# Kernel tuning notes

Hardware: AMD Instinct MI355X
Metric: run time of the kernel (lower is better)

The kernel has to match this reference:

```python
import jax, jax.numpy as jnp
import numpy as np

B, N, C = 1, 2048, 1024
H, D = 16, 64          # num_heads, head_dim
S = 8                  # number of frames; tokens per frame = N // S
NEG_INF = jnp.float32(-1e30)  # stand-in for -inf, numerically safe under jit


def setup_inputs() -> dict:
    key = jax.random.key(0)
    ks = jax.random.split(key, 8)
    x = jax.random.normal(ks[0], (B, N, C), dtype=jnp.float32)
    # tokens grouped contiguously by frame (sorted frame ids)
    frame_ids = jnp.repeat(jnp.arange(S, dtype=jnp.int32), N // S)
    is_hub = jax.random.bernoulli(ks[1], 0.05, (N,))
    adj = jax.random.bernoulli(ks[2], 0.25, (S, S))
    adj = adj.at[jnp.arange(S), jnp.arange(S)].set(True)  # frames always see self
    frame_bias = jax.random.normal(ks[3], (S, S), dtype=jnp.float32) * 0.1
    Wqkv = jax.random.normal(ks[4], (C, 3 * C), dtype=jnp.float32) * 0.02
    bqkv = jnp.zeros((3 * C,), dtype=jnp.float32)
    Wproj = jax.random.normal(ks[5], (C, C), dtype=jnp.float32) * 0.02
    bproj = jnp.zeros((C,), dtype=jnp.float32)
    return {"x": x, "frame_ids": frame_ids, "is_hub": is_hub, "adj": adj,
            "frame_bias": frame_bias, "Wqkv": Wqkv, "bqkv": bqkv,
            "Wproj": Wproj, "bproj": bproj}


def reference(x, frame_ids, is_hub, adj, frame_bias, Wqkv, bqkv, Wproj, bproj):
    # qkv projection: (B,N,3C) -> (3,B,H,N,D)
    qkv = (x @ Wqkv + bqkv).reshape(B, N, 3, H, D).transpose(2, 0, 3, 1, 4)
    q, k, v = qkv[0], qkv[1], qkv[2]

    # flex_attention: scores scaled by 1/sqrt(D) BEFORE score_mod
    scores = jnp.einsum("bhnd,bhmd->bhnm", q, k) * (D ** -0.5)

    # score_mod, vectorized over all (qi,kj) pairs:
    fi = frame_ids                                   # (N,)
    allow = adj[fi][:, fi]                           # (N,N) frame adjacency per token pair
    diff_frame = fi[:, None] != fi[None, :]
    hub_block = diff_frame & (is_hub[:, None] | is_hub[None, :])
    allow = allow & ~hub_block                       # mask_hub_tokens=True
    bias = frame_bias[fi][:, fi]                     # soft_mask=True: add frame-level bias

    scores = jnp.where(allow, scores + bias, NEG_INF)  # broadcast over (b,h)
    attn = jax.nn.softmax(scores, axis=-1)
    out = jnp.einsum("bhnm,bhmd->bhnd", attn, v)
    out = out.transpose(0, 2, 1, 3).reshape(B, N, C)
    return out @ Wproj + bproj
```

## Files before the change

### kernel.cpp

```cpp
#include <hip/hip_runtime.h>

#define NTOK 2048
#define CDIM 1024
#define NHEAD 16
#define HDIM 64
#define NFRM 8
#define FTOK 256

typedef unsigned short ushort;
typedef __attribute__((ext_vector_type(8))) short short8;
typedef __attribute__((ext_vector_type(8))) ushort ushort8;
typedef __attribute__((ext_vector_type(4))) ushort ushort4v;
typedef __attribute__((ext_vector_type(4))) float floatx4;

__device__ __forceinline__ ushort f2bf(float f) {
    unsigned int u = __float_as_uint(f);
    return (ushort)((u + 0x7fffu + ((u >> 16) & 1u)) >> 16);
}

__device__ __forceinline__ void gload_lds16(const void* g, void* l) {
    __builtin_amdgcn_global_load_lds(
        (const __attribute__((address_space(1))) unsigned int*)(uintptr_t)g,
        (__attribute__((address_space(3))) unsigned int*)(unsigned int)(uintptr_t)l,
        16, 0, 0);
}

__global__ __launch_bounds__(256)
void prep_kernel(const float* __restrict__ x, ushort* __restrict__ xb,
                 const float* __restrict__ Wqkv, ushort* __restrict__ wqkvT,
                 const float* __restrict__ Wproj, ushort* __restrict__ wprojT)
{
    __shared__ ushort LT[64][72];
    const int b = blockIdx.x, t = threadIdx.x;

    if (b < 2048) {
        int i = b * 256 + t;
        float4 f = ((const float4*)x)[i];
        ushort4v o = { f2bf(f.x), f2bf(f.y), f2bf(f.z), f2bf(f.w) };
        ((ushort4v*)xb)[i] = o;
        return;
    }

    const float* W; ushort* WT; int K, N, n0, k0;
    if (b < 2816) { int idx = b - 2048; W = Wqkv;  WT = wqkvT;  K = 1024; N = 3072;
                    n0 = (idx % 48) * 64; k0 = (idx / 48) * 64; }
    else          { int idx = b - 2816; W = Wproj; WT = wprojT; K = 1024; N = 1024;
                    n0 = (idx & 15) * 64; k0 = (idx >> 4) * 64; }

    const int kr = t >> 4, nc = t & 15;
#pragma unroll
    for (int i = 0; i < 4; ++i) {
        int k = kr + i * 16;
        float4 w4 = *(const float4*)(W + (size_t)(k0 + k) * N + n0 + nc * 4);
        LT[nc*4+0][k] = f2bf(w4.x);
        LT[nc*4+1][k] = f2bf(w4.y);
        LT[nc*4+2][k] = f2bf(w4.z);
        LT[nc*4+3][k] = f2bf(w4.w);
    }
    __syncthreads();
    const int n = t >> 2;
#pragma unroll
    for (int half = 0; half < 2; ++half) {
        int kc = (t & 3) + 4 * half;
        ushort8 v = *(const ushort8*)&LT[n][kc * 8];
        *(ushort8*)(WT + (size_t)(n0 + n) * K + k0 + kc * 8) = v;
    }
}

__global__ __launch_bounds__(256)
void vtrans_kernel(const ushort* __restrict__ v, ushort* __restrict__ vT)
{
    __shared__ ushort LT[64][72];
    const int t = threadIdx.x, h = blockIdx.y, n0 = blockIdx.x * 64;
    {
        const int tok = t >> 2;
#pragma unroll
        for (int half = 0; half < 2; ++half) {
            int dc = (t & 3) + 4 * half;
            ushort8 v8 = *(const ushort8*)(v + ((size_t)h * NTOK + n0 + tok) * HDIM + dc * 8);
#pragma unroll
            for (int j = 0; j < 8; ++j) LT[dc*8 + j][tok] = v8[j];
        }
    }
    __syncthreads();
    {
        const int d = t >> 2;
#pragma unroll
        for (int half = 0; half < 2; ++half) {
            int tc = (t & 3) + 4 * half;
            ushort8 o8 = *(const ushort8*)&LT[d][tc * 8];
            *(ushort8*)(vT + ((size_t)h * HDIM + d) * NTOK + n0 + tc * 8) = o8;
        }
    }
}

__global__ __launch_bounds__(256)
void gemm_bt_kernel(const ushort* __restrict__ A, const ushort* __restrict__ BT,
                    const float* __restrict__ bias, void* __restrict__ out,
                    int M, int N, int K, int mode)
{
    __shared__ ushort As[2][128 * 32];
    __shared__ ushort Bs[2][128 * 32];

    const int t = threadIdx.x;
    const int wave = t >> 6, lane = t & 63;
    const int quad = lane >> 4, l15 = lane & 15;
    const int row0 = blockIdx.y * 128, col0 = blockIdx.x * 128;
    const int wm = (wave >> 1) * 64, wn = (wave & 1) * 64;

    const int sr = lane >> 2;
    const int sc = (lane & 3) * 8;
    const int r0 = wave * 32;

    floatx4 acc[4][4];
#pragma unroll
    for (int i = 0; i < 4; ++i)
#pragma unroll
        for (int j = 0; j < 4; ++j) acc[i][j] = (floatx4){0.f, 0.f, 0.f, 0.f};

    gload_lds16(A  + (size_t)(row0 + r0      + sr) * K + sc, &As[0][ r0       * 32]);
    gload_lds16(A  + (size_t)(row0 + r0 + 16 + sr) * K + sc, &As[0][(r0 + 16) * 32]);
    gload_lds16(BT + (size_t)(col0 + r0      + sr) * K + sc, &Bs[0][ r0       * 32]);
    gload_lds16(BT + (size_t)(col0 + r0 + 16 + sr) * K + sc, &Bs[0][(r0 + 16) * 32]);

    const int nk = K >> 5;
    for (int ki = 0; ki < nk; ++ki) {
        __syncthreads();
        if (ki + 1 < nk) {
            const int kn = (ki + 1) << 5;
            const int b = (ki + 1) & 1;
            gload_lds16(A  + (size_t)(row0 + r0      + sr) * K + kn + sc, &As[b][ r0       * 32]);
            gload_lds16(A  + (size_t)(row0 + r0 + 16 + sr) * K + kn + sc, &As[b][(r0 + 16) * 32]);
            gload_lds16(BT + (size_t)(col0 + r0      + sr) * K + kn + sc, &Bs[b][ r0       * 32]);
            gload_lds16(BT + (size_t)(col0 + r0 + 16 + sr) * K + kn + sc, &Bs[b][(r0 + 16) * 32]);
        }
        const ushort* as = As[ki & 1];
        const ushort* bs = Bs[ki & 1];

        short8 af[4], bfr[4];
#pragma unroll
        for (int i = 0; i < 4; ++i)
            af[i] = *(const short8*)&as[(wm + i * 16 + l15) * 32 + quad * 8];
#pragma unroll
        for (int j = 0; j < 4; ++j)
            bfr[j] = *(const short8*)&bs[(wn + j * 16 + l15) * 32 + quad * 8];
#pragma unroll
        for (int i = 0; i < 4; ++i)
#pragma unroll
            for (int j = 0; j < 4; ++j)
                acc[i][j] = __builtin_amdgcn_mfma_f32_16x16x32_bf16(af[i], bfr[j], acc[i][j], 0, 0, 0);
    }

    if (mode == 0) {
        float* outf = (float*)out;
#pragma unroll
        for (int j = 0; j < 4; ++j) {
            int col = col0 + wn + j * 16 + l15;
            float bb = bias[col];
#pragma unroll
            for (int i = 0; i < 4; ++i) {
                int rowb = row0 + wm + i * 16 + quad * 4;
#pragma unroll
                for (int r = 0; r < 4; ++r)
                    outf[(size_t)(rowb + r) * N + col] = acc[i][j][r] + bb;
            }
        }
    } else {
        ushort* outb = (ushort*)out;
#pragma unroll
        for (int j = 0; j < 4; ++j) {
            int col = col0 + wn + j * 16 + l15;
            float bb = bias[col];
            int part = col >> 10, hh = (col >> 6) & 15, d = col & 63;
            ushort* dst = outb + ((size_t)(part * NHEAD + hh) * NTOK) * HDIM + d;
#pragma unroll
            for (int i = 0; i < 4; ++i) {
                int rowb = row0 + wm + i * 16 + quad * 4;
#pragma unroll
                for (int r = 0; r < 4; ++r)
                    dst[(size_t)(rowb + r) * HDIM] = f2bf(acc[i][j][r] + bb);
            }
        }
    }
}

__global__ __launch_bounds__(64)
void attn_wave_kernel(const ushort* __restrict__ qkvb,
                      const ushort* __restrict__ vTb,
                      const int* __restrict__ frame_ids,
                      const int* __restrict__ is_hub,
                      const int* __restrict__ adj,
                      const float* __restrict__ frame_bias,
                      ushort* __restrict__ attnb)
{
    __shared__ ushort Ps[16 * 72];

    const int lane = threadIdx.x;
    const int quad = lane >> 4, l15 = lane & 15;
    const int b = blockIdx.x;
    const int h = b & 15, q0 = (b >> 4) * 16;

    const ushort* Qg = qkvb + ((size_t)h * NTOK) * HDIM;
    const ushort* Kg = qkvb + ((size_t)(NHEAD + h) * NTOK) * HDIM;
    const ushort* Vg = vTb + ((size_t)h * HDIM) * NTOK;

    short8 aq0 = *(const short8*)(Qg + (size_t)(q0 + l15) * HDIM + quad * 8);
    short8 aq1 = *(const short8*)(Qg + (size_t)(q0 + l15) * HDIM + 32 + quad * 8);

    const int fq = frame_ids[q0];
    unsigned vpack = 0; int nv = 0;
#pragma unroll
    for (int f = 0; f < NFRM; ++f)
        if (adj[fq * NFRM + f]) { vpack |= (unsigned)f << (3 * nv); ++nv; }
    const int ntot = nv * 4;

    int qh[4];
#pragma unroll
    for (int r = 0; r < 4; ++r) qh[r] = is_hub[q0 + quad * 4 + r];

    float lpart[4] = {0.f, 0.f, 0.f, 0.f};
    floatx4 oacc[4];
#pragma unroll
    for (int dt = 0; dt < 4; ++dt) oacc[dt] = (floatx4){0.f, 0.f, 0.f, 0.f};

    auto tile_k0 = [&](int vt) -> int {
        const int fj = (int)((vpack >> (3 * (vt >> 2))) & 7u);
        return fj * FTOK + (vt & 3) * 64;
    };

    auto load_kv = [&](int k0, short8 (&kaX)[4], short8 (&kbX)[4],
                       short8 (&bvX)[4][2], int (&khX)[4]) {
#pragma unroll
        for (int nt = 0; nt < 4; ++nt) {
            const ushort* kp = Kg + (size_t)(k0 + nt * 16 + l15) * HDIM;
            kaX[nt] = *(const short8*)(kp + quad * 8);
            kbX[nt] = *(const short8*)(kp + 32 + quad * 8);
            khX[nt] = is_hub[k0 + nt * 16 + l15];
        }
#pragma unroll
        for (int dt = 0; dt < 4; ++dt) {
            const ushort* vp = Vg + (size_t)(dt * 16 + l15) * NTOK + k0;
            bvX[dt][0] = *(const short8*)(vp + quad * 8);
            bvX[dt][1] = *(const short8*)(vp + 32 + quad * 8);
        }
    };

    auto do_tile = [&](int vt,
                       short8 (&kaC)[4], short8 (&kbC)[4], short8 (&bvC)[4][2], int (&khC)[4],
                       short8 (&kaN)[4], short8 (&kbN)[4], short8 (&bvN)[4][2], int (&khN)[4]) {
        const int fj = (int)((vpack >> (3 * (vt >> 2))) & 7u);
        const float fb = frame_bias[fq * NFRM + fj];
        const bool same = (fj == fq);

        floatx4 s[4];
#pragma unroll
        for (int nt = 0; nt < 4; ++nt) {
            s[nt] = (floatx4){0.f, 0.f, 0.f, 0.f};
            s[nt] = __builtin_amdgcn_mfma_f32_16x16x32_bf16(aq0, kaC[nt], s[nt], 0, 0, 0);
            s[nt] = __builtin_amdgcn_mfma_f32_16x16x32_bf16(aq1, kbC[nt], s[nt], 0, 0, 0);
        }

        if (vt + 1 < ntot) load_kv(tile_k0(vt + 1), kaN, kbN, bvN, khN);

#pragma unroll
        for (int r = 0; r < 4; ++r) {
            float ps = 0.f;
#pragma unroll
            for (int nt = 0; nt < 4; ++nt) {
                bool allow = same || ((qh[r] == 0) && (khC[nt] == 0));
                float sv = allow ? fmaf(s[nt][r], 0.125f, fb) : -1.0e30f;
                float p = __expf(sv);
                ps += p;
                Ps[(quad * 4 + r) * 72 + nt * 16 + l15] = f2bf(p);
            }
            lpart[r] += ps;
        }

        short8 ap0 = *(const short8*)&Ps[l15 * 72 + quad * 8];
        short8 ap1 = *(const short8*)&Ps[l15 * 72 + 32 + quad * 8];
#pragma unroll
        for (int dt = 0; dt < 4; ++dt) {
            oacc[dt] = __builtin_amdgcn_mfma_f32_16x16x32_bf16(ap0, bvC[dt][0], oacc[dt], 0, 0, 0);
            oacc[dt] = __builtin_amdgcn_mfma_f32_16x16x32_bf16(ap1, bvC[dt][1], oacc[dt], 0, 0, 0);
        }
    };

    short8 kaA[4], kbA[4], kaB[4], kbB[4];
    short8 bvA[4][2], bvB[4][2];
    int khA[4], khB[4];
    load_kv(tile_k0(0), kaA, kbA, bvA, khA);

    for (int vt = 0; vt < ntot; vt += 2) {
        do_tile(vt,     kaA, kbA, bvA, khA, kaB, kbB, bvB, khB);
        do_tile(vt + 1, kaB, kbB, bvB, khB, kaA, kbA, bvA, khA);
    }

    float linv[4];
#pragma unroll
    for (int r = 0; r < 4; ++r) {
        float ls = lpart[r];
        ls += __shfl_xor(ls, 1);
        ls += __shfl_xor(ls, 2);
        ls += __shfl_xor(ls, 4);
        ls += __shfl_xor(ls, 8);
        linv[r] = 1.0f / ls;
    }

#pragma unroll
    for (int dt = 0; dt < 4; ++dt) {
        int col = h * HDIM + dt * 16 + l15;
#pragma unroll
        for (int r = 0; r < 4; ++r) {
            int row = q0 + quad * 4 + r;
            attnb[(size_t)row * CDIM + col] = f2bf(oacc[dt][r] * linv[r]);
        }
    }
}

extern "C" void kernel_launch(void* const* d_in, const int* in_sizes, int n_in,
                              void* d_out, int out_size, void* d_ws, size_t ws_size,
                              hipStream_t stream)
{
    const float* x          = (const float*)d_in[0];
    const int*   frame_ids  = (const int*)d_in[1];
    const int*   is_hub     = (const int*)d_in[2];
    const int*   adj        = (const int*)d_in[3];
    const float* frame_bias = (const float*)d_in[4];
    const float* Wqkv       = (const float*)d_in[5];
    const float* bqkv       = (const float*)d_in[6];
    const float* Wproj      = (const float*)d_in[7];
    const float* bproj      = (const float*)d_in[8];
    float* out = (float*)d_out;

    ushort* xb     = (ushort*)d_ws;
    ushort* wqkvT  = xb     + 2097152;
    ushort* wprojT = wqkvT  + 3145728;
    ushort* qkvb   = wprojT + 1048576;
    ushort* vTb    = qkvb   + 6291456;
    ushort* attnb  = vTb    + 2097152;

    prep_kernel<<<dim3(3072), dim3(256), 0, stream>>>(x, xb, Wqkv, wqkvT, Wproj, wprojT);

    gemm_bt_kernel<<<dim3(3 * CDIM / 128, NTOK / 128), dim3(256), 0, stream>>>(
        xb, wqkvT, bqkv, qkvb, NTOK, 3 * CDIM, CDIM, 1);

    vtrans_kernel<<<dim3(NTOK / 64, NHEAD), dim3(256), 0, stream>>>(
        qkvb + (size_t)2 * NHEAD * NTOK * HDIM, vTb);

    attn_wave_kernel<<<dim3(2048), dim3(64), 0, stream>>>(
        qkvb, vTb, frame_ids, is_hub, adj, frame_bias, attnb);

    gemm_bt_kernel<<<dim3(CDIM / 128, NTOK / 128), dim3(256), 0, stream>>>(
        attnb, wprojT, bproj, out, NTOK, CDIM, CDIM, 0);
}
```

Baseline: 171.3 us.

## Split attention KV tiles across four waves per block and bitpack hub flags

```diff
diff --git a/kernel.cpp b/kernel.cpp
--- a/kernel.cpp
+++ b/kernel.cpp
@@ -8,6 +8,7 @@
 #define FTOK 256
 
 typedef unsigned short ushort;
+typedef unsigned long long u64;
 typedef __attribute__((ext_vector_type(8))) short short8;
 typedef __attribute__((ext_vector_type(8))) ushort ushort8;
 typedef __attribute__((ext_vector_type(4))) ushort ushort4v;
@@ -28,7 +29,8 @@
 __global__ __launch_bounds__(256)
 void prep_kernel(const float* __restrict__ x, ushort* __restrict__ xb,
                  const float* __restrict__ Wqkv, ushort* __restrict__ wqkvT,
-                 const float* __restrict__ Wproj, ushort* __restrict__ wprojT)
+                 const float* __restrict__ Wproj, ushort* __restrict__ wprojT,
+                 const int* __restrict__ is_hub, u64* __restrict__ hubmask)
 {
     __shared__ ushort LT[64][72];
     const int b = blockIdx.x, t = threadIdx.x;
@@ -38,6 +40,15 @@
         float4 f = ((const float4*)x)[i];
         ushort4v o = { f2bf(f.x), f2bf(f.y), f2bf(f.z), f2bf(f.w) };
         ((ushort4v*)xb)[i] = o;
+        return;
+    }
+    if (b >= 3072) {
+        if (t < NTOK / 64) {
+            u64 m = 0;
+            for (int j = 0; j < 64; ++j)
+                m |= (u64)(is_hub[t * 64 + j] != 0) << j;
+            hubmask[t] = m;
+        }
         return;
     }
 
@@ -184,18 +195,20 @@
     }
 }
 
-__global__ __launch_bounds__(64)
-void attn_wave_kernel(const ushort* __restrict__ qkvb,
-                      const ushort* __restrict__ vTb,
-                      const int* __restrict__ frame_ids,
-                      const int* __restrict__ is_hub,
-                      const int* __restrict__ adj,
-                      const float* __restrict__ frame_bias,
-                      ushort* __restrict__ attnb)
-{
-    __shared__ ushort Ps[16 * 72];
-
-    const int lane = threadIdx.x;
+__global__ __launch_bounds__(256)
+void attn_split_kernel(const ushort* __restrict__ qkvb,
+                       const ushort* __restrict__ vTb,
+                       const int* __restrict__ frame_ids,
+                       const u64* __restrict__ hubmask,
+                       const int* __restrict__ adj,
+                       const float* __restrict__ frame_bias,
+                       ushort* __restrict__ attnb)
+{
+    __shared__ float SH[4 * 16 * 68 + 64];
+    ushort* PsAll = (ushort*)SH;
+
+    const int t = threadIdx.x;
+    const int wave = t >> 6, lane = t & 63;
     const int quad = lane >> 4, l15 = lane & 15;
     const int b = blockIdx.x;
     const int h = b & 15, q0 = (b >> 4) * 16;
@@ -203,6 +216,7 @@
     const ushort* Qg = qkvb + ((size_t)h * NTOK) * HDIM;
     const ushort* Kg = qkvb + ((size_t)(NHEAD + h) * NTOK) * HDIM;
     const ushort* Vg = vTb + ((size_t)h * HDIM) * NTOK;
+    ushort* Ps = PsAll + wave * (16 * 72);
 
     short8 aq0 = *(const short8*)(Qg + (size_t)(q0 + l15) * HDIM + quad * 8);
     short8 aq1 = *(const short8*)(Qg + (size_t)(q0 + l15) * HDIM + 32 + quad * 8);
@@ -212,62 +226,45 @@
 #pragma unroll
     for (int f = 0; f < NFRM; ++f)
         if (adj[fq * NFRM + f]) { vpack |= (unsigned)f << (3 * nv); ++nv; }
-    const int ntot = nv * 4;
-
+
+    const u64 hmq = hubmask[q0 >> 6] >> (q0 & 63);
     int qh[4];
 #pragma unroll
-    for (int r = 0; r < 4; ++r) qh[r] = is_hub[q0 + quad * 4 + r];
+    for (int r = 0; r < 4; ++r) qh[r] = (int)((hmq >> (quad * 4 + r)) & 1);
 
     float lpart[4] = {0.f, 0.f, 0.f, 0.f};
     floatx4 oacc[4];
 #pragma unroll
     for (int dt = 0; dt < 4; ++dt) oacc[dt] = (floatx4){0.f, 0.f, 0.f, 0.f};
 
-    auto tile_k0 = [&](int vt) -> int {
-        const int fj = (int)((vpack >> (3 * (vt >> 2))) & 7u);
-        return fj * FTOK + (vt & 3) * 64;
-    };
-
-    auto load_kv = [&](int k0, short8 (&kaX)[4], short8 (&kbX)[4],
-                       short8 (&bvX)[4][2], int (&khX)[4]) {
+    for (int i = 0; i < nv; ++i) {
+        const int fj = (int)((vpack >> (3 * i)) & 7u);
+        const int k0 = fj * FTOK + wave * 64;
+        const float fb = frame_bias[fq * NFRM + fj];
+        const bool same = (fj == fq);
+        const u64 hmk = hubmask[k0 >> 6];
+
+        floatx4 s[4];
 #pragma unroll
         for (int nt = 0; nt < 4; ++nt) {
             const ushort* kp = Kg + (size_t)(k0 + nt * 16 + l15) * HDIM;
-            kaX[nt] = *(const short8*)(kp + quad * 8);
-            kbX[nt] = *(const short8*)(kp + 32 + quad * 8);
-            khX[nt] = is_hub[k0 + nt * 16 + l15];
-        }
-#pragma unroll
-        for (int dt = 0; dt < 4; ++dt) {
-            const ushort* vp = Vg + (size_t)(dt * 16 + l15) * NTOK + k0;
-            bvX[dt][0] = *(const short8*)(vp + quad * 8);
-            bvX[dt][1] = *(const short8*)(vp + 32 + quad * 8);
-        }
-    };
-
-    auto do_tile = [&](int vt,
-                       short8 (&kaC)[4], short8 (&kbC)[4], short8 (&bvC)[4][2], int (&khC)[4],
-                       short8 (&kaN)[4], short8 (&kbN)[4], short8 (&bvN)[4][2], int (&khN)[4]) {
-        const int fj = (int)((vpack >> (3 * (vt >> 2))) & 7u);
-        const float fb = frame_bias[fq * NFRM + fj];
-        const bool same = (fj == fq);
-
-        floatx4 s[4];
-#pragma unroll
-        for (int nt = 0; nt < 4; ++nt) {
+            short8 bk0 = *(const short8*)(kp + quad * 8);
+            short8 bk1 = *(const short8*)(kp + 32 + quad * 8);
             s[nt] = (floatx4){0.f, 0.f, 0.f, 0.f};
-            s[nt] = __builtin_amdgcn_mfma_f32_16x16x32_bf16(aq0, kaC[nt], s[nt], 0, 0, 0);
-            s[nt] = __builtin_amdgcn_mfma_f32_16x16x32_bf16(aq1, kbC[nt], s[nt], 0, 0, 0);
-        }
-
-        if (vt + 1 < ntot) load_kv(tile_k0(vt + 1), kaN, kbN, bvN, khN);
+            s[nt] = __builtin_amdgcn_mfma_f32_16x16x32_bf16(aq0, bk0, s[nt], 0, 0, 0);
+            s[nt] = __builtin_amdgcn_mfma_f32_16x16x32_bf16(aq1, bk1, s[nt], 0, 0, 0);
+        }
+
+        int kh[4];
+#pragma unroll
+        for (int nt = 0; nt < 4; ++nt) kh[nt] = (int)((hmk >> (nt * 16 + l15)) & 1);
 
 #pragma unroll
         for (int r = 0; r < 4; ++r) {
             float ps = 0.f;
 #pragma unroll
             for (int nt = 0; nt < 4; ++nt) {
-                bool allow = same || ((qh[r] == 0) && (khC[nt] == 0));
+                bool allow = same || ((qh[r] == 0) && (kh[nt] == 0));
                 float sv = allow ? fmaf(s[nt][r], 0.125f, fb) : -1.0e30f;
                 float p = __expf(sv);
                 ps += p;
@@ -280,22 +277,14 @@
         short8 ap1 = *(const short8*)&Ps[l15 * 72 + 32 + quad * 8];
 #pragma unroll
         for (int dt = 0; dt < 4; ++dt) {
-            oacc[dt] = __builtin_amdgcn_mfma_f32_16x16x32_bf16(ap0, bvC[dt][0], oacc[dt], 0, 0, 0);
-            oacc[dt] = __builtin_amdgcn_mfma_f32_16x16x32_bf16(ap1, bvC[dt][1], oacc[dt], 0, 0, 0);
-        }
-    };
-
-    short8 kaA[4], kbA[4], kaB[4], kbB[4];
-    short8 bvA[4][2], bvB[4][2];
-    int khA[4], khB[4];
-    load_kv(tile_k0(0), kaA, kbA, bvA, khA);
-
-    for (int vt = 0; vt < ntot; vt += 2) {
-        do_tile(vt,     kaA, kbA, bvA, khA, kaB, kbB, bvB, khB);
-        do_tile(vt + 1, kaB, kbB, bvB, khB, kaA, kbA, bvA, khA);
-    }
-
-    float linv[4];
+            const ushort* vp = Vg + (size_t)(dt * 16 + l15) * NTOK + k0;
+            short8 bv0 = *(const short8*)(vp + quad * 8);
+            short8 bv1 = *(const short8*)(vp + 32 + quad * 8);
+            oacc[dt] = __builtin_amdgcn_mfma_f32_16x16x32_bf16(ap0, bv0, oacc[dt], 0, 0, 0);
+            oacc[dt] = __builtin_amdgcn_mfma_f32_16x16x32_bf16(ap1, bv1, oacc[dt], 0, 0, 0);
+        }
+    }
+
 #pragma unroll
     for (int r = 0; r < 4; ++r) {
         float ls = lpart[r];
@@ -303,17 +292,36 @@
         ls += __shfl_xor(ls, 2);
         ls += __shfl_xor(ls, 4);
         ls += __shfl_xor(ls, 8);
-        linv[r] = 1.0f / ls;
-    }
-
-#pragma unroll
-    for (int dt = 0; dt < 4; ++dt) {
-        int col = h * HDIM + dt * 16 + l15;
-#pragma unroll
-        for (int r = 0; r < 4; ++r) {
-            int row = q0 + quad * 4 + r;
-            attnb[(size_t)row * CDIM + col] = f2bf(oacc[dt][r] * linv[r]);
-        }
+        lpart[r] = ls;
+    }
+
+    __syncthreads();
+
+#pragma unroll
+    for (int dt = 0; dt < 4; ++dt)
+#pragma unroll
+        for (int r = 0; r < 4; ++r)
+            SH[(wave * 16 + quad * 4 + r) * 68 + dt * 16 + l15] = oacc[dt][r];
+    if (l15 == 0)
+#pragma unroll
+        for (int r = 0; r < 4; ++r)
+            SH[4 * 16 * 68 + wave * 16 + quad * 4 + r] = lpart[r];
+
+    __syncthreads();
+
+    {
+        const int row = t >> 4, cg = (t & 15) * 4;
+        float4 o = {0.f, 0.f, 0.f, 0.f};
+        float l = 0.f;
+#pragma unroll
+        for (int w = 0; w < 4; ++w) {
+            float4 ow = *(const float4*)&SH[(w * 16 + row) * 68 + cg];
+            o.x += ow.x; o.y += ow.y; o.z += ow.z; o.w += ow.w;
+            l += SH[4 * 16 * 68 + w * 16 + row];
+        }
+        float li = 1.0f / l;
+        ushort4v ob = { f2bf(o.x * li), f2bf(o.y * li), f2bf(o.z * li), f2bf(o.w * li) };
+        *(ushort4v*)(attnb + (size_t)(q0 + row) * CDIM + h * HDIM + cg) = ob;
     }
 }
 
@@ -338,8 +346,10 @@
     ushort* qkvb   = wprojT + 1048576;
     ushort* vTb    = qkvb   + 6291456;
     ushort* attnb  = vTb    + 2097152;
-
-    prep_kernel<<<dim3(3072), dim3(256), 0, stream>>>(x, xb, Wqkv, wqkvT, Wproj, wprojT);
+    u64*    hubmask = (u64*)(attnb + 2097152);
+
+    prep_kernel<<<dim3(3073), dim3(256), 0, stream>>>(
+        x, xb, Wqkv, wqkvT, Wproj, wprojT, is_hub, hubmask);
 
     gemm_bt_kernel<<<dim3(3 * CDIM / 128, NTOK / 128), dim3(256), 0, stream>>>(
         xb, wqkvT, bqkv, qkvb, NTOK, 3 * CDIM, CDIM, 1);
@@ -347,8 +357,8 @@
     vtrans_kernel<<<dim3(NTOK / 64, NHEAD), dim3(256), 0, stream>>>(
         qkvb + (size_t)2 * NHEAD * NTOK * HDIM, vTb);
 
-    attn_wave_kernel<<<dim3(2048), dim3(64), 0, stream>>>(
-        qkvb, vTb, frame_ids, is_hub, adj, frame_bias, attnb);
+    attn_split_kernel<<<dim3(2048), dim3(256), 0, stream>>>(
+        qkvb, vTb, frame_ids, hubmask, adj, frame_bias, attnb);
 
     gemm_bt_kernel<<<dim3(CDIM / 128, NTOK / 128), dim3(256), 0, stream>>>(
         attnb, wprojT, bproj, out, NTOK, CDIM, CDIM, 0);
```

Result: no change. 173.4 us (+1.3%).
